# Optimization experiments

Hardware: AMD Instinct MI355X
Metric: run time of the kernel (lower is better)

The kernel has to match this reference:

```python
import jax, jax.numpy as jnp
import numpy as np
import math

IN_SIZE = 4096
OUT_SIZE = 4096
NNZ = 4_194_304
BATCH = 4096


def setup_inputs() -> dict:
    key = jax.random.key(0)
    k_x, k_v, k_i, k_o = jax.random.split(key, 4)
    x = jax.random.normal(k_x, (BATCH, IN_SIZE), dtype=jnp.float32)
    # v = randn(nnz) * (6 / sqrt(in_size + out_size))  (init=None branch)
    scale = 6.0 / math.sqrt(IN_SIZE + OUT_SIZE)
    values = jax.random.normal(k_v, (NNZ,), dtype=jnp.float32) * scale
    idx_in = jax.random.randint(k_i, (NNZ,), 0, IN_SIZE, dtype=jnp.int64 if jax.config.jax_enable_x64 else jnp.int32)
    idx_out = jax.random.randint(k_o, (NNZ,), 0, OUT_SIZE, dtype=jnp.int64 if jax.config.jax_enable_x64 else jnp.int32)
    return {"x": x, "values": values, "idx_in": idx_in, "idx_out": idx_out}


def reference(x, values, idx_in, idx_out):
    # torch.sparse.mm(W, x.T).T with W = coo((idx_out, idx_in), values, (out, in)).
    # Duplicate (row,col) entries in COO sum, which x.at[...].add reproduces.
    # Scattering into a dense [out, in] matrix (64 MB) is the efficient JAX form;
    # it avoids any [nnz, batch] intermediate and then uses one dense GEMM.
    W = jnp.zeros((OUT_SIZE, IN_SIZE), dtype=values.dtype).at[idx_out, idx_in].add(values)
    return x @ W.T  # [batch, out_size]
```

## Files before the change

### kernel.cpp

```cpp
#include <hip/hip_runtime.h>
#include <hip/hip_bf16.h>

#define IN_SIZE 4096
#define OUT_SIZE 4096
#define BATCH 4096

#define NBLK 512
#define CHUNK 8192
#define NCELL 1024
#define CELLCAP 8192

typedef __bf16 bf16x8 __attribute__((ext_vector_type(8)));
typedef float f32x4 __attribute__((ext_vector_type(4)));

__global__ __launch_bounds__(256) void zero_kernel(int* __restrict__ cellcnt) {
    cellcnt[blockIdx.x * 256 + threadIdx.x & 1023] = 0;
}

__global__ __launch_bounds__(512) void scatres_kernel(const float* __restrict__ vals,
                                                      const int* __restrict__ iin,
                                                      const int* __restrict__ iout,
                                                      int* __restrict__ cellcnt,
                                                      uint2* __restrict__ bkt, int nnz) {
    __shared__ int sout[CHUNK];
    __shared__ int hist[NCELL];
    __shared__ int gbase[NCELL];
    const int b = blockIdx.x, tid = threadIdx.x;
    const int base = b * CHUNK;

    for (int c = tid; c < NCELL; c += 512) hist[c] = 0;
    __syncthreads();

    const int4* io4 = (const int4*)(iout + base);
    for (int i = tid; i < CHUNK / 4; i += 512) {
        if (base + i * 4 + 3 < nnz) {
            const int4 o = io4[i];
            ((int4*)sout)[i] = o;
            atomicAdd(&hist[o.x >> 2], 1);
            atomicAdd(&hist[o.y >> 2], 1);
            atomicAdd(&hist[o.z >> 2], 1);
            atomicAdd(&hist[o.w >> 2], 1);
        } else {
            for (int j = 0; j < 4; ++j) {
                const int k = base + i * 4 + j;
                if (k < nnz) {
                    const int o = iout[k];
                    sout[i * 4 + j] = o;
                    atomicAdd(&hist[o >> 2], 1);
                }
            }
        }
    }
    __syncthreads();

    for (int c = tid; c < NCELL; c += 512)
        gbase[c] = hist[c] ? atomicAdd(&cellcnt[c], hist[c]) : 0;
    __syncthreads();

    const float4* v4 = (const float4*)(vals + base);
    const int4*   a4 = (const int4*)(iin + base);
    for (int i = tid; i < CHUNK / 4; i += 512) {
        if (base + i * 4 + 3 < nnz) {
            const float4 v = v4[i];
            const int4   a = a4[i];
            const int4   o = ((const int4*)sout)[i];
            int c, l; uint2 e;
            c = o.x >> 2; l = atomicSub(&hist[c], 1) - 1;
            e.x = __builtin_bit_cast(unsigned, v.x); e.y = (unsigned)(((o.x & 3) << 12) | a.x);
            bkt[(size_t)c * CELLCAP + gbase[c] + l] = e;
            c = o.y >> 2; l = atomicSub(&hist[c], 1) - 1;
            e.x = __builtin_bit_cast(unsigned, v.y); e.y = (unsigned)(((o.y & 3) << 12) | a.y);
            bkt[(size_t)c * CELLCAP + gbase[c] + l] = e;
            c = o.z >> 2; l = atomicSub(&hist[c], 1) - 1;
            e.x = __builtin_bit_cast(unsigned, v.z); e.y = (unsigned)(((o.z & 3) << 12) | a.z);
            bkt[(size_t)c * CELLCAP + gbase[c] + l] = e;
            c = o.w >> 2; l = atomicSub(&hist[c], 1) - 1;
            e.x = __builtin_bit_cast(unsigned, v.w); e.y = (unsigned)(((o.w & 3) << 12) | a.w);
            bkt[(size_t)c * CELLCAP + gbase[c] + l] = e;
        } else {
            for (int j = 0; j < 4; ++j) {
                const int k = base + i * 4 + j;
                if (k < nnz) {
                    const int o = sout[i * 4 + j];
                    const int c = o >> 2;
                    const int l = atomicSub(&hist[c], 1) - 1;
                    uint2 e;
                    e.x = __builtin_bit_cast(unsigned, vals[k]);
                    e.y = (unsigned)(((o & 3) << 12) | iin[k]);
                    bkt[(size_t)c * CELLCAP + gbase[c] + l] = e;
                }
            }
        }
    }
}

__global__ __launch_bounds__(512) void accum_kernel(const uint2* __restrict__ bkt,
                                                    const int* __restrict__ cellcnt,
                                                    __bf16* __restrict__ W,
                                                    const f32x4* __restrict__ xin,
                                                    bf16x8* __restrict__ xout) {
    __shared__ float acc[4 * 4096];
    const int cell = blockIdx.x, tid = threadIdx.x;
    for (int t = tid; t < 4 * 4096; t += 512) acc[t] = 0.f;
    int n = cellcnt[cell];
    if (n > CELLCAP) n = CELLCAP;
    __syncthreads();

    const uint2* seg = bkt + (size_t)cell * CELLCAP;
    for (int s = tid; s < n; s += 512) {
        const uint2 e = seg[s];
        atomicAdd(&acc[((e.y >> 12) & 3u) * 4096 + (e.y & 0xFFFu)],
                  __builtin_bit_cast(float, e.x));
    }
    __syncthreads();

    bf16x8* out = (bf16x8*)(W + (size_t)cell * 4 * 4096);
    for (int t = tid; t < 2048; t += 512) {
        bf16x8 o;
#pragma unroll
        for (int j = 0; j < 8; ++j) o[j] = (__bf16)acc[t * 8 + j];
        out[t] = o;
    }

    const int xbase = blockIdx.x * 2048;
    for (int t = tid; t < 2048; t += 512) {
        const int idx = xbase + t;
        const f32x4 a = xin[2 * idx];
        const f32x4 bq = xin[2 * idx + 1];
        bf16x8 o;
        o[0] = (__bf16)a[0];  o[1] = (__bf16)a[1];  o[2] = (__bf16)a[2];  o[3] = (__bf16)a[3];
        o[4] = (__bf16)bq[0]; o[5] = (__bf16)bq[1]; o[6] = (__bf16)bq[2]; o[7] = (__bf16)bq[3];
        xout[idx] = o;
    }
}

#define GNT 128

#define STAGE_A(T)                                                            \
  do {                                                                        \
    const __bf16* s_ = gA0 + (size_t)(T) * 32;                                \
    __bf16* d_ = &smem[((T) & 3) * 16384 + tid * 8];                          \
    __builtin_amdgcn_global_load_lds(                                         \
        (const __attribute__((address_space(1))) void*)s_,                    \
        (__attribute__((address_space(3))) void*)d_, 16, 0, 0);               \
    __builtin_amdgcn_global_load_lds(                                         \
        (const __attribute__((address_space(1))) void*)(s_ + (size_t)524288), \
        (__attribute__((address_space(3))) void*)(d_ + 4096), 16, 0, 0);      \
  } while (0)

#define STAGE_B(T)                                                            \
  do {                                                                        \
    const __bf16* s_ = gB0 + (size_t)(T) * 32;                                \
    __bf16* d_ = &smem[((T) & 3) * 16384 + 8192 + tid * 8];                   \
    __builtin_amdgcn_global_load_lds(                                         \
        (const __attribute__((address_space(1))) void*)s_,                    \
        (__attribute__((address_space(3))) void*)d_, 16, 0, 0);               \
    __builtin_amdgcn_global_load_lds(                                         \
        (const __attribute__((address_space(1))) void*)(s_ + (size_t)524288), \
        (__attribute__((address_space(3))) void*)(d_ + 4096), 16, 0, 0);      \
  } while (0)

#define VMW8 asm volatile("s_waitcnt vmcnt(8)" ::: "memory")
#define VMW4 asm volatile("s_waitcnt vmcnt(4)" ::: "memory")
#define VMW0 asm volatile("s_waitcnt vmcnt(0)" ::: "memory")
#define VMWN ((void)0)

#define GTILE(T, DOSTAGE, VMWAIT, ENDBAR)                                     \
  do {                                                                        \
    const __bf16* bp_ = &smem[((T) & 3) * 16384];                             \
    bf16x8 bfr_[4], af_[4];                                                   \
    _Pragma("unroll") for (int j_ = 0; j_ < 4; ++j_)                          \
        bfr_[j_] = *(const bf16x8*)(bp_ + offB[j_]);                          \
    _Pragma("unroll") for (int i_ = 0; i_ < 4; ++i_)                          \
        af_[i_] = *(const bf16x8*)(bp_ + offA[i_]);                           \
    if (DOSTAGE) STAGE_A((T) + 3);                                            \
    __builtin_amdgcn_s_barrier();                                             \
    __builtin_amdgcn_s_setprio(1);                                            \
    _Pragma("unroll") for (int i_ = 0; i_ < 4; ++i_)                          \
        _Pragma("unroll") for (int j_ = 0; j_ < 4; ++j_)                      \
            acc[i_][j_] = __builtin_amdgcn_mfma_f32_16x16x32_bf16(            \
                af_[i_], bfr_[j_], acc[i_][j_], 0, 0, 0);                     \
    __builtin_amdgcn_s_setprio(0);                                            \
    __builtin_amdgcn_s_barrier();                                             \
    _Pragma("unroll") for (int i_ = 0; i_ < 4; ++i_)                          \
        af_[i_] = *(const bf16x8*)(bp_ + offA[4 + i_]);                       \
    if (DOSTAGE) STAGE_B((T) + 3);                                            \
    __builtin_amdgcn_s_barrier();                                             \
    __builtin_amdgcn_s_setprio(1);                                            \
    _Pragma("unroll") for (int i_ = 0; i_ < 4; ++i_)                          \
        _Pragma("unroll") for (int j_ = 0; j_ < 4; ++j_)                      \
            acc[4 + i_][j_] = __builtin_amdgcn_mfma_f32_16x16x32_bf16(        \
                af_[i_], bfr_[j_], acc[4 + i_][j_], 0, 0, 0);                 \
    __builtin_amdgcn_s_setprio(0);                                            \
    asm volatile("s_waitcnt lgkmcnt(0)" ::: "memory");                        \
    VMWAIT;                                                                   \
    if (ENDBAR) __builtin_amdgcn_s_barrier();                                 \
  } while (0)

__global__ __launch_bounds__(512, 2) void gemm_bt_kernel(
    const __bf16* __restrict__ A,
    const __bf16* __restrict__ B,
    float* __restrict__ C) {
    __shared__ __bf16 smem[4 * 16384];

    const int tid   = threadIdx.x;
    const int lane  = tid & 63;
    const int wv    = tid >> 6;
    const int wm    = wv >> 2;
    const int wn    = wv & 3;
    const int row16 = lane & 15;
    const int quad  = lane >> 4;

    const int swz = (blockIdx.x & 7) * 32 + (blockIdx.x >> 3);
    const int bm  = (swz >> 4) * 256;
    const int bn  = (swz & 15) * 256;

    const int sr = tid >> 2;
    const int sq = (tid & 3) ^ ((sr >> 1) & 3);
    const __bf16* gA0 = A + (size_t)(bm + sr) * 4096 + sq * 8;
    const __bf16* gB0 = B + (size_t)(bn + sr) * 4096 + sq * 8;

    int offA[8], offB[4];
#pragma unroll
    for (int i = 0; i < 8; ++i) {
        const int ra = wm * 128 + i * 16 + row16;
        offA[i] = ra * 32 + ((quad ^ ((ra >> 1) & 3)) * 8);
    }
#pragma unroll
    for (int j = 0; j < 4; ++j) {
        const int rb = wn * 64 + j * 16 + row16;
        offB[j] = 8192 + rb * 32 + ((quad ^ ((rb >> 1) & 3)) * 8);
    }

    f32x4 acc[8][4] = {};

    STAGE_A(0); STAGE_B(0);
    STAGE_A(1); STAGE_B(1);
    STAGE_A(2); STAGE_B(2);
    VMW8;
    __builtin_amdgcn_s_barrier();

    int t = 0;
    for (; t < GNT - 3; ++t) GTILE(t, true, VMW8, true);
    GTILE(t, false, VMW4, true); ++t;
    GTILE(t, false, VMW0, true); ++t;
    GTILE(t, false, VMWN, false);

#pragma unroll
    for (int i = 0; i < 8; ++i) {
        const int rbase = bm + wm * 128 + i * 16 + quad * 4;
#pragma unroll
        for (int j = 0; j < 4; ++j) {
            const int col = bn + wn * 64 + j * 16 + row16;
#pragma unroll
            for (int r = 0; r < 4; ++r)
                C[(size_t)(rbase + r) * 4096 + col] = acc[i][j][r];
        }
    }
}

extern "C" void kernel_launch(void* const* d_in, const int* in_sizes, int n_in,
                              void* d_out, int out_size, void* d_ws, size_t ws_size,
                              hipStream_t stream) {
    const float* x    = (const float*)d_in[0];
    const float* vals = (const float*)d_in[1];
    const int*   iin  = (const int*)d_in[2];
    const int*   iout = (const int*)d_in[3];
    float*       C    = (float*)d_out;
    const int    nnz  = in_sizes[1];

    char*   ws      = (char*)d_ws;
    __bf16* Wb      = (__bf16*)ws;
    __bf16* Xb      = (__bf16*)(ws + ((size_t)32 << 20));
    int*    cellcnt = (int*)(ws + ((size_t)64 << 20));
    uint2*  bkt     = (uint2*)d_out;

    zero_kernel<<<4, 256, 0, stream>>>(cellcnt);
    scatres_kernel<<<NBLK, 512, 0, stream>>>(vals, iin, iout, cellcnt, bkt, nnz);
    accum_kernel<<<NCELL, 512, 0, stream>>>(bkt, cellcnt, Wb, (const f32x4*)x, (bf16x8*)Xb);
    gemm_bt_kernel<<<256, 512, 0, stream>>>(Xb, Wb, C);
}
```

Baseline: 344.2 us.

## Double-buffer LDS fragments in registers and cut per-tile barriers in GEMM loop

```diff
diff --git a/kernel.cpp b/kernel.cpp
--- a/kernel.cpp
+++ b/kernel.cpp
@@ -134,67 +134,66 @@
     }
 }
 
-#define GNT 128
-
-#define STAGE_A(T)                                                            \
+
+#define GLL(SRC, DST)                                                         \
+    __builtin_amdgcn_global_load_lds(                                         \
+        (const __attribute__((address_space(1))) void*)(SRC),                 \
+        (__attribute__((address_space(3))) void*)(DST), 16, 0, 0)
+
+#define STAGE_AB(T, BUF)                                                      \
   do {                                                                        \
-    const __bf16* s_ = gA0 + (size_t)(T) * 32;                                \
-    __bf16* d_ = &smem[((T) & 3) * 16384 + tid * 8];                          \
-    __builtin_amdgcn_global_load_lds(                                         \
-        (const __attribute__((address_space(1))) void*)s_,                    \
-        (__attribute__((address_space(3))) void*)d_, 16, 0, 0);               \
-    __builtin_amdgcn_global_load_lds(                                         \
-        (const __attribute__((address_space(1))) void*)(s_ + (size_t)524288), \
-        (__attribute__((address_space(3))) void*)(d_ + 4096), 16, 0, 0);      \
+    const __bf16* sa_ = gA0 + (size_t)(T) * 32;                               \
+    __bf16* da_ = &smem[(BUF) * 16384 + tid * 8];                             \
+    GLL(sa_, da_);                                                            \
+    GLL(sa_ + (size_t)524288, da_ + 4096);                                    \
+    const __bf16* sb_ = gB0 + (size_t)(T) * 32;                               \
+    __bf16* db_ = &smem[(BUF) * 16384 + 8192 + tid * 8];                      \
+    GLL(sb_, db_);                                                            \
+    GLL(sb_ + (size_t)524288, db_ + 4096);                                    \
   } while (0)
 
-#define STAGE_B(T)                                                            \
-  do {                                                                        \
-    const __bf16* s_ = gB0 + (size_t)(T) * 32;                                \
-    __bf16* d_ = &smem[((T) & 3) * 16384 + 8192 + tid * 8];                   \
-    __builtin_amdgcn_global_load_lds(                                         \
-        (const __attribute__((address_space(1))) void*)s_,                    \
-        (__attribute__((address_space(3))) void*)d_, 16, 0, 0);               \
-    __builtin_amdgcn_global_load_lds(                                         \
-        (const __attribute__((address_space(1))) void*)(s_ + (size_t)524288), \
-        (__attribute__((address_space(3))) void*)(d_ + 4096), 16, 0, 0);      \
-  } while (0)
-
-#define VMW8 asm volatile("s_waitcnt vmcnt(8)" ::: "memory")
-#define VMW4 asm volatile("s_waitcnt vmcnt(4)" ::: "memory")
-#define VMW0 asm volatile("s_waitcnt vmcnt(0)" ::: "memory")
-#define VMWN ((void)0)
-
-#define GTILE(T, DOSTAGE, VMWAIT, ENDBAR)                                     \
-  do {                                                                        \
-    const __bf16* bp_ = &smem[((T) & 3) * 16384];                             \
-    bf16x8 bfr_[4], af_[4];                                                   \
+#define VMW8  asm volatile("s_waitcnt vmcnt(8)" ::: "memory")
+#define VMW4  asm volatile("s_waitcnt vmcnt(4)" ::: "memory")
+#define VMW0  asm volatile("s_waitcnt vmcnt(0)" ::: "memory")
+#define VMWN  ((void)0)
+#define LGKM0 asm volatile("s_waitcnt lgkmcnt(0)" ::: "memory")
+
+#define LBFR(D, BUF)                                                          \
     _Pragma("unroll") for (int j_ = 0; j_ < 4; ++j_)                          \
-        bfr_[j_] = *(const bf16x8*)(bp_ + offB[j_]);                          \
-    _Pragma("unroll") for (int i_ = 0; i_ < 4; ++i_)                          \
-        af_[i_] = *(const bf16x8*)(bp_ + offA[i_]);                           \
-    if (DOSTAGE) STAGE_A((T) + 3);                                            \
-    __builtin_amdgcn_s_barrier();                                             \
-    __builtin_amdgcn_s_setprio(1);                                            \
+        D[j_] = *(const bf16x8*)(smem + (BUF) * 16384 + offB[j_])
+#define LA03(D, BUF)                                                          \
+    _Pragma("unroll") for (int i_ = 0; i_ < 4; ++i_)                          \
+        D[i_] = *(const bf16x8*)(smem + (BUF) * 16384 + offA[i_])
+#define LA47(BUF)                                                             \
+    _Pragma("unroll") for (int i_ = 0; i_ < 4; ++i_)                          \
+        af47[i_] = *(const bf16x8*)(smem + (BUF) * 16384 + offA[4 + i_])
+
+#define MFMA_C1(CA, CB)                                                       \
     _Pragma("unroll") for (int i_ = 0; i_ < 4; ++i_)                          \
         _Pragma("unroll") for (int j_ = 0; j_ < 4; ++j_)                      \
             acc[i_][j_] = __builtin_amdgcn_mfma_f32_16x16x32_bf16(            \
-                af_[i_], bfr_[j_], acc[i_][j_], 0, 0, 0);                     \
-    __builtin_amdgcn_s_setprio(0);                                            \
-    __builtin_amdgcn_s_barrier();                                             \
-    _Pragma("unroll") for (int i_ = 0; i_ < 4; ++i_)                          \
-        af_[i_] = *(const bf16x8*)(bp_ + offA[4 + i_]);                       \
-    if (DOSTAGE) STAGE_B((T) + 3);                                            \
-    __builtin_amdgcn_s_barrier();                                             \
-    __builtin_amdgcn_s_setprio(1);                                            \
+                CA[i_], CB[j_], acc[i_][j_], 0, 0, 0)
+#define MFMA_C2(CB)                                                           \
     _Pragma("unroll") for (int i_ = 0; i_ < 4; ++i_)                          \
         _Pragma("unroll") for (int j_ = 0; j_ < 4; ++j_)                      \
             acc[4 + i_][j_] = __builtin_amdgcn_mfma_f32_16x16x32_bf16(        \
-                af_[i_], bfr_[j_], acc[4 + i_][j_], 0, 0, 0);                 \
+                af47[i_], CB[j_], acc[4 + i_][j_], 0, 0, 0)
+
+#define ITER(T, BUFC, BUFN, CB, CA, NB, NA, DOSTAGE, SBUF, VMW, DOBAR)        \
+  do {                                                                        \
+    if (DOSTAGE) STAGE_AB((T) + 3, SBUF);                                     \
+    LA47(BUFC);                                                               \
+    __builtin_amdgcn_s_setprio(1);                                            \
+    MFMA_C1(CA, CB);                                                          \
     __builtin_amdgcn_s_setprio(0);                                            \
-    asm volatile("s_waitcnt lgkmcnt(0)" ::: "memory");                        \
-    VMWAIT;                                                                   \
-    if (ENDBAR) __builtin_amdgcn_s_barrier();                                 \
+    LBFR(NB, BUFN);                                                           \
+    LA03(NA, BUFN);                                                           \
+    __builtin_amdgcn_s_setprio(1);                                            \
+    MFMA_C2(CB);                                                              \
+    __builtin_amdgcn_s_setprio(0);                                            \
+    LGKM0;                                                                    \
+    VMW;                                                                      \
+    if (DOBAR) __builtin_amdgcn_s_barrier();                                  \
   } while (0)
 
 __global__ __launch_bounds__(512, 2) void gemm_bt_kernel(
@@ -232,19 +231,30 @@
         offB[j] = 8192 + rb * 32 + ((quad ^ ((rb >> 1) & 3)) * 8);
     }
 
-    f32x4 acc[8][4] = {};
-
-    STAGE_A(0); STAGE_B(0);
-    STAGE_A(1); STAGE_B(1);
-    STAGE_A(2); STAGE_B(2);
-    VMW8;
+    f32x4  acc[8][4] = {};
+    bf16x8 bfr0[4], a0_[4], bfr1[4], a1_[4], af47[4];
+
+    STAGE_AB(0, 0); STAGE_AB(1, 1); STAGE_AB(2, 2);
+    VMW4;
     __builtin_amdgcn_s_barrier();
-
-    int t = 0;
-    for (; t < GNT - 3; ++t) GTILE(t, true, VMW8, true);
-    GTILE(t, false, VMW4, true); ++t;
-    GTILE(t, false, VMW0, true); ++t;
-    GTILE(t, false, VMWN, false);
+    LBFR(bfr0, 0);
+    LA03(a0_, 0);
+
+    for (int c = 0; c < 31; ++c) {
+        const int tb = c * 4;
+        ITER(tb + 0, 0, 1, bfr0, a0_, bfr1, a1_, 1, 3, VMW4, 1);
+        ITER(tb + 1, 1, 2, bfr1, a1_, bfr0, a0_, 1, 0, VMW4, 1);
+        ITER(tb + 2, 2, 3, bfr0, a0_, bfr1, a1_, 1, 1, VMW4, 1);
+        ITER(tb + 3, 3, 0, bfr1, a1_, bfr0, a0_, 1, 2, VMW4, 1);
+    }
+    ITER(124, 0, 1, bfr0, a0_, bfr1, a1_, 1, 3, VMW4, 1);
+    ITER(125, 1, 2, bfr1, a1_, bfr0, a0_, 0, 0, VMW0, 1);
+    ITER(126, 2, 3, bfr0, a0_, bfr1, a1_, 0, 0, VMWN, 0);
+    LA47(3);
+    __builtin_amdgcn_s_setprio(1);
+    MFMA_C1(a1_, bfr1);
+    MFMA_C2(bfr1);
+    __builtin_amdgcn_s_setprio(0);
 
 #pragma unroll
     for (int i = 0; i < 8; ++i) {
```

New measurement: 350.3 us. Within noise of the previous version (+1.8%).
